# Kernel tuning notes

Hardware: AMD Instinct MI355X
Metric: run time of the kernel (lower is better)

Reference implementation:

```python
import jax, jax.numpy as jnp
import numpy as np

N = 10000   # nodes
E = 100000  # edges
B = 64      # graphs
HID = 128


def setup_inputs() -> dict:
    key = jax.random.key(0)
    ks = iter(jax.random.split(key, 64))
    def nrm(shape, s=0.1):
        return jax.random.normal(next(ks), shape, dtype=jnp.float32) * s
    inp = {}
    inp["x"] = nrm((N, 1), 1.0)
    inp["node_type"] = jax.random.randint(next(ks), (N,), 0, 2)
    inp["edge_index"] = jax.random.randint(next(ks), (2, E), 0, N)
    inp["edge_attr"] = nrm((E, 1), 1.0)
    inp["batch"] = jnp.sort(jax.random.randint(next(ks), (N,), 0, B))
    inp["vp_w"] = nrm((1, HID)); inp["vp_b"] = nrm((HID,))
    inp["type_emb"] = nrm((2, HID))
    def conv(pre, fin, h, c):
        inp[pre + "_wl"] = nrm((fin, h * c)); inp[pre + "_bl"] = nrm((h * c,))
        inp[pre + "_wr"] = nrm((fin, h * c)); inp[pre + "_br"] = nrm((h * c,))
        inp[pre + "_we"] = nrm((1, h * c));  inp[pre + "_att"] = nrm((h, c))
        inp[pre + "_bias"] = nrm((h * c if pre != "c3" else c,))
    conv("c1", HID, 8, HID)
    conv("c2", HID * 8, 2, HID)
    conv("c3", HID * 2, 1, HID)
    inp["m1_w"] = nrm((HID, HID)); inp["m1_b"] = nrm((HID,))
    inp["ln1_g"] = jnp.ones((HID,), jnp.float32); inp["ln1_b"] = jnp.zeros((HID,), jnp.float32)
    inp["m2_w"] = nrm((HID, HID // 2)); inp["m2_b"] = nrm((HID // 2,))
    inp["ln2_g"] = jnp.ones((HID // 2,), jnp.float32); inp["ln2_b"] = jnp.zeros((HID // 2,), jnp.float32)
    inp["m3_w"] = nrm((HID // 2, 1)); inp["m3_b"] = nrm((1,))
    return inp


def _gatv2(x, src, dst, ea, wl, bl, wr, br, we, att, bias, heads, out_ch, concat):
    """PyG GATv2Conv (eval mode): add self-loops (edge_attr fill='mean' over dst),
    attn = (att * leaky_relu(Wl x_src + Wr x_dst + We e)).sum(-1), segment-softmax
    over destination, scatter-add of alpha * Wl x_src."""
    n = x.shape[0]
    ones = jnp.ones((ea.shape[0], 1), ea.dtype)
    deg = jax.ops.segment_sum(ones, dst, num_segments=n)
    loop_attr = jax.ops.segment_sum(ea, dst, num_segments=n) / jnp.maximum(deg, 1.0)
    ar = jnp.arange(n, dtype=src.dtype)
    src2 = jnp.concatenate([src, ar])
    dst2 = jnp.concatenate([dst, ar])
    ea2 = jnp.concatenate([ea, loop_attr], axis=0)
    xl = (x @ wl + bl).reshape(n, heads, out_ch)   # source transform
    xr = (x @ wr + br).reshape(n, heads, out_ch)   # target transform
    e = (ea2 @ we).reshape(-1, heads, out_ch)      # [E2, H, C]
    msg = xl[src2]                                 # [E2, H, C]
    z = jax.nn.leaky_relu(msg + xr[dst2] + e, 0.2)
    score = jnp.einsum('ehc,hc->eh', z, att)       # [E2, H]
    smax = jax.ops.segment_max(score, dst2, num_segments=n)
    ex = jnp.exp(score - smax[dst2])
    denom = jax.ops.segment_sum(ex, dst2, num_segments=n)
    alpha = ex / denom[dst2]
    out = jax.ops.segment_sum(alpha[:, :, None] * msg, dst2, num_segments=n)
    out = out.reshape(n, heads * out_ch) if concat else out.mean(axis=1)
    return out + bias


def _layernorm(v, g, b):
    mu = v.mean(-1, keepdims=True)
    var = v.var(-1, keepdims=True)
    return (v - mu) / jnp.sqrt(var + 1e-5) * g + b


def reference(x, node_type, edge_index, edge_attr, batch,
              vp_w, vp_b, type_emb,
              c1_wl, c1_bl, c1_wr, c1_br, c1_we, c1_att, c1_bias,
              c2_wl, c2_bl, c2_wr, c2_br, c2_we, c2_att, c2_bias,
              c3_wl, c3_bl, c3_wr, c3_br, c3_we, c3_att, c3_bias,
              m1_w, m1_b, ln1_g, ln1_b, m2_w, m2_b, ln2_g, ln2_b, m3_w, m3_b):
    src, dst = edge_index[0], edge_index[1]
    h = x @ vp_w + vp_b + type_emb[node_type]
    h = jax.nn.leaky_relu(_gatv2(h, src, dst, edge_attr, c1_wl, c1_bl, c1_wr, c1_br, c1_we, c1_att, c1_bias, 8, HID, True), 0.2)
    h = jax.nn.leaky_relu(_gatv2(h, src, dst, edge_attr, c2_wl, c2_bl, c2_wr, c2_br, c2_we, c2_att, c2_bias, 2, HID, True), 0.2)
    h = jax.nn.leaky_relu(_gatv2(h, src, dst, edge_attr, c3_wl, c3_bl, c3_wr, c3_br, c3_we, c3_att, c3_bias, 1, HID, False), 0.2)
    # masked global mean pool over node_type == 0
    w = (node_type == 0).astype(h.dtype)
    sums = jax.ops.segment_sum(h * w[:, None], batch, num_segments=B)
    cnts = jax.ops.segment_sum(w, batch, num_segments=B)
    pooled = sums / jnp.maximum(cnts, 1.0)[:, None]
    h1 = jax.nn.leaky_relu(_layernorm(pooled @ m1_w + m1_b, ln1_g, ln1_b), 0.2)
    h2 = jax.nn.leaky_relu(_layernorm(h1 @ m2_w + m2_b, ln2_g, ln2_b), 0.2)
    return (h2 @ m3_w + m3_b).squeeze(-1)
```

## Files before the change

### kernel.cpp

```cpp
#include <hip/hip_runtime.h>
#include <math.h>

#define NN 10000
#define NE 100000
#define NBATCH 64

typedef short bf16x8 __attribute__((ext_vector_type(8)));
typedef float f32x4 __attribute__((ext_vector_type(4)));

__device__ __forceinline__ float lrelu(float v){ return v > 0.f ? v : 0.2f*v; }

__device__ __forceinline__ unsigned short f2bf(float x){
  unsigned int u = __float_as_uint(x);
  u += 0x7fffu + ((u >> 16) & 1u);
  return (unsigned short)(u >> 16);
}
__device__ __forceinline__ float bf2f(unsigned short u){
  return __uint_as_float(((unsigned int)u) << 16);
}

__global__ __launch_bounds__(256) void prep_kernel(
    const float* __restrict__ vp_w, const float* __restrict__ vp_b,
    const float* __restrict__ type_emb,
    const float* __restrict__ c1_wl, const float* __restrict__ c1_bl,
    const float* __restrict__ c1_wr, const float* __restrict__ c1_br,
    float* __restrict__ Ul, float* __restrict__ CTl,
    float* __restrict__ Ur, float* __restrict__ CTr,
    const float* __restrict__ c2_wl, const float* __restrict__ c2_wr,
    const float* __restrict__ c3_wl, const float* __restrict__ c3_wr,
    unsigned short* __restrict__ W2lT, unsigned short* __restrict__ W2rT,
    unsigned short* __restrict__ W3lT, unsigned short* __restrict__ W3rT,
    float* __restrict__ zbase, int zero_words)
{
  __shared__ float t[64][65];
  int b = blockIdx.x;
  int tid = threadIdx.x;
  if (b < 144){
    const float* in; unsigned short* out; int K, N, idx;
    if (b < 64)      { in=c2_wl; out=W2lT; K=1024; N=256; idx=b; }
    else if (b <128) { in=c2_wr; out=W2rT; K=1024; N=256; idx=b-64; }
    else if (b <136) { in=c3_wl; out=W3lT; K=256;  N=128; idx=b-128; }
    else             { in=c3_wr; out=W3rT; K=256;  N=128; idx=b-136; }
    int K64 = K >> 6;
    int kx = idx % K64, nx = idx / K64;
    int k0 = kx*64, n0 = nx*64;
    int lr = tid >> 4;
    int lc = (tid & 15) * 4;
#pragma unroll
    for (int i=0;i<4;++i){
      int r = lr + i*16;
      float4 v = *(const float4*)(in + (size_t)(k0+r)*N + n0 + lc);
      t[r][lc+0]=v.x; t[r][lc+1]=v.y; t[r][lc+2]=v.z; t[r][lc+3]=v.w;
    }
    __syncthreads();
    int sr = tid >> 3;
    int sc = (tid & 7) * 8;
#pragma unroll
    for (int i=0;i<2;++i){
      int n = sr + i*32;
      unsigned short tmp[8];
#pragma unroll
      for (int j=0;j<8;++j) tmp[j] = f2bf(t[sc+j][n]);
      unsigned short* op = out + (size_t)(n0+n)*K + k0 + sc;
      *(ushort4*)op       = make_ushort4(tmp[0],tmp[1],tmp[2],tmp[3]);
      *(ushort4*)(op + 4) = make_ushort4(tmp[4],tmp[5],tmp[6],tmp[7]);
    }
  } else if (b < 148){
    int j = (b-144)*256 + tid;
    float ul=0.f, c0l=0.f, c1l=0.f, ur=0.f, c0r=0.f, c1r=0.f;
    for (int k=0; k<128; ++k){
      float a = c1_wl[k*1024 + j], bb = c1_wr[k*1024 + j];
      float vw = vp_w[k], vb = vp_b[k], t0 = type_emb[k], t1 = type_emb[128+k];
      ul += vw*a; ur += vw*bb;
      c0l += (vb+t0)*a; c1l += (vb+t1)*a;
      c0r += (vb+t0)*bb; c1r += (vb+t1)*bb;
    }
    Ul[j]=ul; Ur[j]=ur;
    CTl[j]      = c0l + c1_bl[j];
    CTl[1024+j] = c1l + c1_bl[j];
    CTr[j]      = c0r + c1_br[j];
    CTr[1024+j] = c1r + c1_br[j];
  } else {
    for (int i = (b-148)*256 + tid; i < zero_words; i += 32*256)
      zbase[i] = 0.f;
  }
}

__global__ __launch_bounds__(1024) void csr_kernel(
    const int* __restrict__ src, const int* __restrict__ dst, const float* __restrict__ ea,
    int* __restrict__ deg, float* __restrict__ loop_sum,
    int* __restrict__ rowptr, float* __restrict__ loop_attr,
    int* __restrict__ rowctr, int* __restrict__ srcs, float* __restrict__ eav,
    int* __restrict__ sync_)
{
  int tid = threadIdx.x;
  int e = blockIdx.x*1024 + tid;
  int d_ = 0; float eav_ = 0.f;
  bool active = e < NE;
  if (active){
    d_ = dst[e]; eav_ = ea[e];
    atomicAdd(&deg[d_], 1);
    atomicAdd(&loop_sum[d_], eav_);
  }
  __threadfence();
  __syncthreads();
  __shared__ int amlast;
  if (tid == 0) amlast = (atomicAdd(&sync_[0], 1) == (int)gridDim.x - 1);
  __syncthreads();
  if (amlast){
    __shared__ int wsum[16];
    __shared__ int carry_s;
    int lane = tid & 63, wid = tid >> 6;
    if (tid == 0) carry_s = 0;
    __syncthreads();
    for (int base = 0; base < NN; base += 1024){
      int i = base + tid;
      int v = 0; float ls = 0.f;
      if (i < NN){ v = atomicAdd(&deg[i], 0); ls = atomicAdd(&loop_sum[i], 0.f); }
      int incl = v;
#pragma unroll
      for (int off=1; off<64; off<<=1){
        int tt = __shfl_up(incl, off, 64);
        if (lane >= off) incl += tt;
      }
      if (lane == 63) wsum[wid] = incl;
      __syncthreads();
      int pre = carry_s;
      for (int w2=0; w2<wid; ++w2) pre += wsum[w2];
      if (i < NN){
        rowptr[i] = pre + incl - v;
        loop_attr[i] = ls / fmaxf((float)v, 1.f);
      }
      __syncthreads();
      if (tid == 0){
        int t2 = 0;
        for (int w2=0; w2<16; ++w2) t2 += wsum[w2];
        carry_s += t2;
      }
      __syncthreads();
    }
    if (tid == 0) rowptr[NN] = carry_s;
    __threadfence();
    __syncthreads();
    if (tid == 0) atomicExch(&sync_[1], 1);
  }
  if (tid == 0){
    while (atomicAdd(&sync_[1], 0) == 0) __builtin_amdgcn_s_sleep(16);
  }
  __syncthreads();
  if (active){
    int p = atomicAdd(&rowptr[d_], 0) + atomicAdd(&rowctr[d_], 1);
    srcs[p] = src[e];
    eav[p] = eav_;
  }
}

__global__ __launch_bounds__(256) void conv1_kernel(
    const int* __restrict__ rowptr, const int* __restrict__ srcs, const float* __restrict__ eav,
    const float* __restrict__ loop_attr, const float* __restrict__ x, const int* __restrict__ ntype,
    const float* __restrict__ Ul, const float* __restrict__ CTl,
    const float* __restrict__ Ur, const float* __restrict__ CTr,
    const float* __restrict__ we, const float* __restrict__ att, const float* __restrict__ bias,
    unsigned short* __restrict__ out)
{
  int n = blockIdx.x;
  int tid = threadIdx.x;
  int ch0 = tid * 4;
  float wev[4], atv[4], biv[4], ulv[4], c0l[4], c1l[4], xrv[4];
  {
    float urv[4], c0r[4], c1r[4];
#pragma unroll
    for (int v=0; v<4; ++v){
      int ch = ch0 + v;
      wev[v] = we[ch]; atv[v] = att[ch]; biv[v] = bias[ch];
      ulv[v] = Ul[ch]; c0l[v] = CTl[ch]; c1l[v] = CTl[1024+ch];
      urv[v] = Ur[ch]; c0r[v] = CTr[ch]; c1r[v] = CTr[1024+ch];
    }
    float xn = x[n];
    int tn = ntype[n];
#pragma unroll
    for (int v=0; v<4; ++v) xrv[v] = xn*urv[v] + (tn ? c1r[v] : c0r[v]);
  }
  float m0=-INFINITY, l0=0.f, A0[4]={0.f,0.f,0.f,0.f};
  float m1=-INFINITY, l1=0.f, A1[4]={0.f,0.f,0.f,0.f};
  int beg = rowptr[n], end = rowptr[n+1];
  for (int j = beg; j <= end; j += 2){
    bool two = (j+1) <= end;
    int s0 = (j < end) ? srcs[j] : n;
    float e0 = (j < end) ? eav[j] : loop_attr[n];
    int s1 = n; float e1 = 0.f;
    if (two){ s1 = (j+1 < end) ? srcs[j+1] : n; e1 = (j+1 < end) ? eav[j+1] : loop_attr[n]; }
    float xs0 = x[s0]; int ts0 = ntype[s0];
    float xs1 = 0.f; int ts1 = 0;
    if (two){ xs1 = x[s1]; ts1 = ntype[s1]; }
    float xl0[4], xl1[4];
#pragma unroll
    for (int v=0; v<4; ++v){
      xl0[v] = xs0*ulv[v] + (ts0 ? c1l[v] : c0l[v]);
      xl1[v] = xs1*ulv[v] + (ts1 ? c1l[v] : c0l[v]);
    }
    float p0 = 0.f, p1 = 0.f;
#pragma unroll
    for (int v=0; v<4; ++v){
      p0 += atv[v]*lrelu(xl0[v] + xrv[v] + e0*wev[v]);
      p1 += atv[v]*lrelu(xl1[v] + xrv[v] + e1*wev[v]);
    }
#pragma unroll
    for (int mm=1; mm<32; mm<<=1){
      p0 += __shfl_xor(p0, mm, 64);
      p1 += __shfl_xor(p1, mm, 64);
    }
    {
      float mn = fmaxf(m0, p0), sc = __expf(m0-mn), pe = __expf(p0-mn);
      l0 = l0*sc + pe; m0 = mn;
#pragma unroll
      for (int v=0; v<4; ++v) A0[v] = A0[v]*sc + pe*xl0[v];
    }
    if (two){
      float mn = fmaxf(m1, p1), sc = __expf(m1-mn), pe = __expf(p1-mn);
      l1 = l1*sc + pe; m1 = mn;
#pragma unroll
      for (int v=0; v<4; ++v) A1[v] = A1[v]*sc + pe*xl1[v];
    }
  }
  float mn = fmaxf(m0, m1);
  float sc0 = __expf(m0-mn), sc1 = __expf(m1-mn);
  float inv = 1.f/(l0*sc0 + l1*sc1);
  size_t baseo = (size_t)n*1024 + ch0;
  ushort4 o;
  o.x = f2bf(lrelu((A0[0]*sc0 + A1[0]*sc1)*inv + biv[0]));
  o.y = f2bf(lrelu((A0[1]*sc0 + A1[1]*sc1)*inv + biv[1]));
  o.z = f2bf(lrelu((A0[2]*sc0 + A1[2]*sc1)*inv + biv[2]));
  o.w = f2bf(lrelu((A0[3]*sc0 + A1[3]*sc1)*inv + biv[3]));
  *(ushort4*)(out + baseo) = o;
}

template<int H, int THREADS, int VPT, bool ONLY0, bool OUTBF, bool INBF>
__global__ __launch_bounds__(THREADS) void conv_kernel(
    const int* __restrict__ rowptr, const int* __restrict__ srcs, const float* __restrict__ eav,
    const float* __restrict__ loop_attr, const int* __restrict__ ntype,
    const void* __restrict__ Xv, int stride, int xr_off,
    const float* __restrict__ we, const float* __restrict__ att, const float* __restrict__ bias,
    void* __restrict__ out)
{
  const int HC = THREADS*VPT;
  const int TPH = THREADS/H;
  int n = blockIdx.x;
  if (ONLY0 && ntype[n] != 0) return;
  int tid = threadIdx.x;
  int ch0 = tid * VPT;
  const float* Xf = (const float*)Xv;
  const unsigned short* Xb = (const unsigned short*)Xv;
  float wev[VPT], atv[VPT], biv[VPT], xrv[VPT];
#pragma unroll
  for (int v=0; v<VPT; ++v){
    int ch = ch0+v;
    wev[v]=we[ch]; atv[v]=att[ch]; biv[v]=bias[ch];
  }
  if constexpr (INBF){
    ushort4 q = *(const ushort4*)(Xb + (size_t)n*stride + xr_off + ch0);
    xrv[0]=bf2f(q.x); xrv[1]=bf2f(q.y); xrv[2]=bf2f(q.z); xrv[3]=bf2f(q.w);
  } else {
#pragma unroll
    for (int v=0; v<VPT; ++v) xrv[v]=Xf[(size_t)n*stride + xr_off + ch0+v];
  }
  float m0=-INFINITY, l0=0.f, A0[VPT];
  float m1=-INFINITY, l1=0.f, A1[VPT];
#pragma unroll
  for (int v=0; v<VPT; ++v){ A0[v]=0.f; A1[v]=0.f; }
  int beg=rowptr[n], end=rowptr[n+1];
  for (int j=beg; j<=end; j+=2){
    bool two = (j+1) <= end;
    int s0 = (j < end) ? srcs[j] : n;
    float e0 = (j < end) ? eav[j] : loop_attr[n];
    int s1 = n; float e1 = 0.f;
    if (two){ s1 = (j+1 < end) ? srcs[j+1] : n; e1 = (j+1 < end) ? eav[j+1] : loop_attr[n]; }
    float x0[VPT], x1[VPT];
    if constexpr (INBF){
      ushort4 q0 = *(const ushort4*)(Xb + (size_t)s0*stride + ch0);
      x0[0]=bf2f(q0.x); x0[1]=bf2f(q0.y); x0[2]=bf2f(q0.z); x0[3]=bf2f(q0.w);
      if (two){
        ushort4 q1 = *(const ushort4*)(Xb + (size_t)s1*stride + ch0);
        x1[0]=bf2f(q1.x); x1[1]=bf2f(q1.y); x1[2]=bf2f(q1.z); x1[3]=bf2f(q1.w);
      } else { x1[0]=x1[1]=x1[2]=x1[3]=0.f; }
    } else if constexpr (VPT == 4){
      float4 q0 = *(const float4*)(Xf + (size_t)s0*stride + ch0);
      x0[0]=q0.x; x0[1]=q0.y; x0[2]=q0.z; x0[3]=q0.w;
      if (two){
        float4 q1 = *(const float4*)(Xf + (size_t)s1*stride + ch0);
        x1[0]=q1.x; x1[1]=q1.y; x1[2]=q1.z; x1[3]=q1.w;
      } else { x1[0]=x1[1]=x1[2]=x1[3]=0.f; }
    } else {
      float2 q0 = *(const float2*)(Xf + (size_t)s0*stride + ch0);
      x0[0]=q0.x; x0[1]=q0.y;
      if (two){
        float2 q1 = *(const float2*)(Xf + (size_t)s1*stride + ch0);
        x1[0]=q1.x; x1[1]=q1.y;
      } else { x1[0]=x1[1]=0.f; }
    }
    float p0=0.f, p1=0.f;
#pragma unroll
    for (int v=0; v<VPT; ++v){
      p0 += atv[v]*lrelu(x0[v]+xrv[v]+e0*wev[v]);
      p1 += atv[v]*lrelu(x1[v]+xrv[v]+e1*wev[v]);
    }
#pragma unroll
    for (int mm=1; mm<TPH; mm<<=1){
      p0 += __shfl_xor(p0, mm, 64);
      p1 += __shfl_xor(p1, mm, 64);
    }
    {
      float mn=fmaxf(m0,p0), sc=__expf(m0-mn), pe=__expf(p0-mn);
      l0=l0*sc+pe; m0=mn;
#pragma unroll
      for (int v=0; v<VPT; ++v) A0[v]=A0[v]*sc+pe*x0[v];
    }
    if (two){
      float mn=fmaxf(m1,p1), sc=__expf(m1-mn), pe=__expf(p1-mn);
      l1=l1*sc+pe; m1=mn;
#pragma unroll
      for (int v=0; v<VPT; ++v) A1[v]=A1[v]*sc+pe*x1[v];
    }
  }
  float mn = fmaxf(m0, m1);
  float sc0 = __expf(m0-mn), sc1 = __expf(m1-mn);
  float inv = 1.f/(l0*sc0 + l1*sc1);
  size_t baseo=(size_t)n*HC+ch0;
  if constexpr (OUTBF){
    unsigned short* ob = (unsigned short*)out;
    ushort4 o;
    o.x = f2bf(lrelu((A0[0]*sc0+A1[0]*sc1)*inv+biv[0]));
    o.y = f2bf(lrelu((A0[1]*sc0+A1[1]*sc1)*inv+biv[1]));
    o.z = f2bf(lrelu((A0[2]*sc0+A1[2]*sc1)*inv+biv[2]));
    o.w = f2bf(lrelu((A0[3]*sc0+A1[3]*sc1)*inv+biv[3]));
    *(ushort4*)(ob + baseo) = o;
  } else {
    float* of = (float*)out;
#pragma unroll
    for (int v=0; v<VPT; ++v) of[baseo+v]=lrelu((A0[v]*sc0+A1[v]*sc1)*inv+biv[v]);
  }
}

template<bool OUTBF>
__global__ __launch_bounds__(256) void gemm_dual_lds(
    const short* __restrict__ Abf,
    const short* __restrict__ WlT, const short* __restrict__ WrT,
    const float* __restrict__ bl, const float* __restrict__ br,
    void* __restrict__ Out, int M, int K, int NcH, int cgrid, int rgrid)
{
  __shared__ short lds[12288];
  int id = blockIdx.x;
  int xcd = id & 7, slot = id >> 3;
  int nb = slot % cgrid;
  int rowgroup = (slot / cgrid) * 8 + xcd;
  if (rowgroup >= rgrid) return;
  int row0 = rowgroup * 128;
  int NC2 = 2*NcH;
  int halfx = NcH >> 6;
  int isR = nb >= halfx;
  const short* WT = isR ? WrT : WlT;
  const float* bias = isR ? br : bl;
  int col0 = (nb - (isR ? halfx : 0)) * 64;
  int gcol0 = nb * 64;
  int tid = threadIdx.x;
  int lane = tid & 63, wave = tid >> 6;
  int wm = wave >> 1, wn = wave & 1;
  int quad = lane >> 4, l16 = lane & 15;

  const short* asrc[4];
#pragma unroll
  for (int i=0;i<4;++i){
    int c = wave*256 + i*64 + lane;
    int m = c >> 3, j = c & 7;
    int gr = row0 + m; gr = gr < M ? gr : M-1;
    asrc[i] = Abf + (size_t)gr*K + ((j ^ (m & 7)) << 3);
  }
  const short* bsrc[2];
#pragma unroll
  for (int i=0;i<2;++i){
    int c = wave*128 + i*64 + lane;
    int nloc = c >> 3, j = c & 7;
    bsrc[i] = WT + (size_t)(col0 + nloc)*K + ((j ^ (nloc & 7)) << 3);
  }

  float biasv[2] = { bias[col0 + wn*32 + l16], bias[col0 + wn*32 + 16 + l16] };
  f32x4 acc[4][2];
#pragma unroll
  for (int f=0; f<4; ++f)
#pragma unroll
    for (int g=0; g<2; ++g) acc[f][g] = (f32x4){0.f,0.f,0.f,0.f};

  int niter = K >> 6;
  for (int it=0; it<niter; ++it){
    int k0 = it << 6;
#pragma unroll
    for (int i=0;i<4;++i)
      __builtin_amdgcn_global_load_lds(asrc[i] + k0, &lds[(wave*256 + i*64)*8], 16, 0, 0);
#pragma unroll
    for (int i=0;i<2;++i)
      __builtin_amdgcn_global_load_lds(bsrc[i] + k0, &lds[8192 + (wave*128 + i*64)*8], 16, 0, 0);
    __syncthreads();
#pragma unroll
    for (int s=0; s<2; ++s){
      int t = s*4 + quad;
      bf16x8 af[4], bfv[2];
#pragma unroll
      for (int f=0; f<4; ++f){
        int m = wm*64 + f*16 + l16;
        af[f] = *(const bf16x8*)&lds[m*64 + ((t ^ (m & 7)) << 3)];
      }
#pragma unroll
      for (int g=0; g<2; ++g){
        int nloc = wn*32 + g*16 + l16;
        bfv[g] = *(const bf16x8*)&lds[8192 + nloc*64 + ((t ^ (nloc & 7)) << 3)];
      }
#pragma unroll
      for (int f=0; f<4; ++f)
#pragma unroll
        for (int g=0; g<2; ++g)
          acc[f][g] = __builtin_amdgcn_mfma_f32_16x16x32_bf16(af[f], bfv[g], acc[f][g], 0,0,0);
    }
    __syncthreads();
  }

#pragma unroll
  for (int f=0; f<4; ++f){
    int rbase = row0 + wm*64 + f*16 + quad*4;
#pragma unroll
    for (int r=0; r<4; ++r){
      int rr = rbase + r;
      if (rr < M){
#pragma unroll
        for (int g=0; g<2; ++g){
          int cc = gcol0 + wn*32 + g*16 + l16;
          float val = acc[f][g][r] + biasv[g];
          if constexpr (OUTBF) ((unsigned short*)Out)[(size_t)rr*NC2 + cc] = f2bf(val);
          else                 ((float*)Out)[(size_t)rr*NC2 + cc] = val;
        }
      }
    }
  }
}

__device__ __forceinline__ int lbound(const int* __restrict__ a, int n, int key){
  int lo = 0, hi = n;
  while (lo < hi){ int mid = (lo+hi) >> 1; if (a[mid] < key) lo = mid+1; else hi = mid; }
  return lo;
}

__global__ __launch_bounds__(128) void head_kernel(
    const float* __restrict__ h3, const int* __restrict__ ntype, const int* __restrict__ batch,
    const float* __restrict__ m1w, const float* __restrict__ m1b,
    const float* __restrict__ g1, const float* __restrict__ b1,
    const float* __restrict__ m2w, const float* __restrict__ m2b,
    const float* __restrict__ g2, const float* __restrict__ b2,
    const float* __restrict__ m3w, const float* __restrict__ m3b,
    float* __restrict__ out)
{
  __shared__ float p[128];
  __shared__ float hb[128];
  __shared__ float red[128];
  int b = blockIdx.x, j = threadIdx.x;
  int lo = lbound(batch, NN, b);
  int hi = lbound(batch, NN, b+1);
  float s = 0.f, cnt = 0.f;
  int n = lo;
  for (; n + 3 < hi; n += 4){
    float w0 = (ntype[n]   == 0) ? 1.f : 0.f;
    float w1 = (ntype[n+1] == 0) ? 1.f : 0.f;
    float w2 = (ntype[n+2] == 0) ? 1.f : 0.f;
    float w3 = (ntype[n+3] == 0) ? 1.f : 0.f;
    s += w0*h3[(size_t)n*128 + j]     + w1*h3[(size_t)(n+1)*128 + j]
       + w2*h3[(size_t)(n+2)*128 + j] + w3*h3[(size_t)(n+3)*128 + j];
    cnt += w0 + w1 + w2 + w3;
  }
  for (; n < hi; ++n){
    float w = (ntype[n] == 0) ? 1.f : 0.f;
    s += w*h3[(size_t)n*128 + j];
    cnt += w;
  }
  p[j] = s / fmaxf(cnt, 1.f);
  __syncthreads();
  float a = m1b[j];
  for (int k=0; k<128; ++k) a += p[k]*m1w[k*128 + j];
  red[j] = a; __syncthreads();
  for (int off=64; off>0; off>>=1){ if (j<off) red[j] += red[j+off]; __syncthreads(); }
  float mu = red[0] * (1.f/128.f);
  __syncthreads();
  float d = a - mu;
  red[j] = d*d; __syncthreads();
  for (int off=64; off>0; off>>=1){ if (j<off) red[j] += red[j+off]; __syncthreads(); }
  float var = red[0] * (1.f/128.f);
  __syncthreads();
  hb[j] = lrelu(d * rsqrtf(var + 1e-5f) * g1[j] + b1[j]);
  __syncthreads();
  float a2 = 0.f;
  if (j < 64){
    a2 = m2b[j];
    for (int k=0; k<128; ++k) a2 += hb[k]*m2w[k*64 + j];
  }
  red[j] = (j<64) ? a2 : 0.f; __syncthreads();
  for (int off=64; off>0; off>>=1){ if (j<off) red[j] += red[j+off]; __syncthreads(); }
  float mu2 = red[0] * (1.f/64.f);
  __syncthreads();
  float d2 = a2 - mu2;
  red[j] = (j<64) ? d2*d2 : 0.f; __syncthreads();
  for (int off=64; off>0; off>>=1){ if (j<off) red[j] += red[j+off]; __syncthreads(); }
  float var2 = red[0] * (1.f/64.f);
  __syncthreads();
  if (j < 64) hb[j] = lrelu(d2 * rsqrtf(var2 + 1e-5f) * g2[j] + b2[j]);
  __syncthreads();
  if (j == 0){
    float o = m3b[0];
    for (int k=0; k<64; ++k) o += hb[k]*m3w[k];
    out[b] = o;
  }
}

extern "C" void kernel_launch(void* const* d_in, const int* in_sizes, int n_in,
                              void* d_out, int out_size, void* d_ws, size_t ws_size,
                              hipStream_t stream)
{
  const float* x        = (const float*)d_in[0];
  const int*   ntype    = (const int*)d_in[1];
  const int*   ei       = (const int*)d_in[2];
  const float* eattr    = (const float*)d_in[3];
  const int*   batch    = (const int*)d_in[4];
  const float* vp_w     = (const float*)d_in[5];
  const float* vp_b     = (const float*)d_in[6];
  const float* type_emb = (const float*)d_in[7];
  const float* c1_wl = (const float*)d_in[8];  const float* c1_bl = (const float*)d_in[9];
  const float* c1_wr = (const float*)d_in[10]; const float* c1_br = (const float*)d_in[11];
  const float* c1_we = (const float*)d_in[12]; const float* c1_att= (const float*)d_in[13];
  const float* c1_bias=(const float*)d_in[14];
  const float* c2_wl = (const float*)d_in[15]; const float* c2_bl = (const float*)d_in[16];
  const float* c2_wr = (const float*)d_in[17]; const float* c2_br = (const float*)d_in[18];
  const float* c2_we = (const float*)d_in[19]; const float* c2_att= (const float*)d_in[20];
  const float* c2_bias=(const float*)d_in[21];
  const float* c3_wl = (const float*)d_in[22]; const float* c3_bl = (const float*)d_in[23];
  const float* c3_wr = (const float*)d_in[24]; const float* c3_br = (const float*)d_in[25];
  const float* c3_we = (const float*)d_in[26]; const float* c3_att= (const float*)d_in[27];
  const float* c3_bias=(const float*)d_in[28];
  const float* m1_w = (const float*)d_in[29]; const float* m1_b = (const float*)d_in[30];
  const float* ln1_g= (const float*)d_in[31]; const float* ln1_b= (const float*)d_in[32];
  const float* m2_w = (const float*)d_in[33]; const float* m2_b = (const float*)d_in[34];
  const float* ln2_g= (const float*)d_in[35]; const float* ln2_b= (const float*)d_in[36];
  const float* m3_w = (const float*)d_in[37]; const float* m3_b = (const float*)d_in[38];
  const int* esrc = ei;
  const int* edst = ei + NE;
  float* outp = (float*)d_out;
  (void)in_sizes; (void)n_in; (void)out_size; (void)ws_size;

  char* w = (char*)d_ws;
  auto alloc = [&](size_t bytes) -> void* {
    void* p = (void*)w;
    w += (bytes + 255) & ~(size_t)255;
    return p;
  };
  unsigned short* h1bf = (unsigned short*)alloc((size_t)NN*1024*2);
  unsigned short* X2   = (unsigned short*)alloc((size_t)NN*512*2);
  unsigned short* h2bf = (unsigned short*)alloc((size_t)NN*256*2);
  float* X3   = (float*)alloc((size_t)NN*256*4);
  float* h3   = (float*)alloc((size_t)NN*128*4);
  unsigned short* W2lT = (unsigned short*)alloc((size_t)256*1024*2);
  unsigned short* W2rT = (unsigned short*)alloc((size_t)256*1024*2);
  unsigned short* W3lT = (unsigned short*)alloc((size_t)128*256*2);
  unsigned short* W3rT = (unsigned short*)alloc((size_t)128*256*2);
  float* Ul   = (float*)alloc(1024*4);
  float* CTl  = (float*)alloc(2048*4);
  float* Ur   = (float*)alloc(1024*4);
  float* CTr  = (float*)alloc(2048*4);
  const int zero_words = 3*NN + 2;
  float* zbase = (float*)alloc((size_t)zero_words*4);
  int*   deg      = (int*)zbase;
  int*   rowctr   = (int*)(zbase + NN);
  float* loop_sum = zbase + 2*NN;
  int*   sync_    = (int*)(zbase + 3*NN);
  float* loop_attr= (float*)alloc((size_t)NN*4);
  int*   rowptr   = (int*)alloc((size_t)(NN+1)*4);
  int*   srcs     = (int*)alloc((size_t)NE*4);
  float* eav      = (float*)alloc((size_t)NE*4);

  prep_kernel<<<180, 256, 0, stream>>>(vp_w, vp_b, type_emb,
      c1_wl, c1_bl, c1_wr, c1_br, Ul, CTl, Ur, CTr,
      c2_wl, c2_wr, c3_wl, c3_wr, W2lT, W2rT, W3lT, W3rT,
      zbase, zero_words);
  csr_kernel<<<(NE+1023)/1024, 1024, 0, stream>>>(esrc, edst, eattr,
      deg, loop_sum, rowptr, loop_attr, rowctr, srcs, eav, sync_);
  conv1_kernel<<<NN, 256, 0, stream>>>(rowptr, srcs, eav, loop_attr, x, ntype,
                                       Ul, CTl, Ur, CTr, c1_we, c1_att, c1_bias, h1bf);
  gemm_dual_lds<true><<<640, 256, 0, stream>>>(
      (const short*)h1bf, (const short*)W2lT, (const short*)W2rT, c2_bl, c2_br,
      (void*)X2, NN, 1024, 256, 8, 79);
  conv_kernel<2,64,4,false,true,true><<<NN, 64, 0, stream>>>(rowptr, srcs, eav, loop_attr, ntype,
      (const void*)X2, 512, 256, c2_we, c2_att, c2_bias, h2bf);
  gemm_dual_lds<false><<<320, 256, 0, stream>>>(
      (const short*)h2bf, (const short*)W3lT, (const short*)W3rT, c3_bl, c3_br,
      (void*)X3, NN, 256, 128, 4, 79);
  conv_kernel<1,64,2,true,false,false><<<NN, 64, 0, stream>>>(rowptr, srcs, eav, loop_attr, ntype,
      (const void*)X3, 256, 128, c3_we, c3_att, c3_bias, h3);
  head_kernel<<<NBATCH, 128, 0, stream>>>(h3, ntype, batch, m1_w, m1_b, ln1_g, ln1_b,
                                          m2_w, m2_b, ln2_g, ln2_b, m3_w, m3_b, outp);
}
```

Baseline: 359.1 us.

## Split conv1 into edge-parallel scoring and per-node softmax aggregation using rank-one structure

Conv1 is split into two kernels. The first computes attention scores for every edge (self-loops included) in an edge-parallel grid, using a precomputed 4-way node-type constant table held in LDS. The second does the per-node, per-head softmax over scalar scores only. Because the first-layer input features are rank-one plus a type constant, the weighted sum reduces to three scalars (sum of alpha times x, and alpha mass per type), which then expand to 1024 channels. This removes the serial per-edge channel loop and its cross-wave reductions, at the cost of writing and reading a 110k×8 score buffer and an extra launch.

```diff
diff --git a/kernel.cpp b/kernel.cpp
--- a/kernel.cpp
+++ b/kernel.cpp
@@ -3,6 +3,7 @@
 
 #define NN 10000
 #define NE 100000
+#define E2 (NE + NN)
 #define NBATCH 64
 
 typedef short bf16x8 __attribute__((ext_vector_type(8)));
@@ -25,7 +26,7 @@
     const float* __restrict__ c1_wl, const float* __restrict__ c1_bl,
     const float* __restrict__ c1_wr, const float* __restrict__ c1_br,
     float* __restrict__ Ul, float* __restrict__ CTl,
-    float* __restrict__ Ur, float* __restrict__ CTr,
+    float* __restrict__ Ur, float* __restrict__ CT2,
     const float* __restrict__ c2_wl, const float* __restrict__ c2_wr,
     const float* __restrict__ c3_wl, const float* __restrict__ c3_wr,
     unsigned short* __restrict__ W2lT, unsigned short* __restrict__ W2rT,
@@ -75,11 +76,14 @@
       c0l += (vb+t0)*a; c1l += (vb+t1)*a;
       c0r += (vb+t0)*bb; c1r += (vb+t1)*bb;
     }
+    float bl = c1_bl[j], br = c1_br[j];
     Ul[j]=ul; Ur[j]=ur;
-    CTl[j]      = c0l + c1_bl[j];
-    CTl[1024+j] = c1l + c1_bl[j];
-    CTr[j]      = c0r + c1_br[j];
-    CTr[1024+j] = c1r + c1_br[j];
+    CTl[j]      = c0l + bl;
+    CTl[1024+j] = c1l + bl;
+    CT2[j]        = (c0l+bl) + (c0r+br);
+    CT2[1024+j]   = (c0l+bl) + (c1r+br);
+    CT2[2048+j]   = (c1l+bl) + (c0r+br);
+    CT2[3072+j]   = (c1l+bl) + (c1r+br);
   } else {
     for (int i = (b-148)*256 + tid; i < zero_words; i += 32*256)
       zbase[i] = 0.f;
@@ -90,8 +94,8 @@
     const int* __restrict__ src, const int* __restrict__ dst, const float* __restrict__ ea,
     int* __restrict__ deg, float* __restrict__ loop_sum,
     int* __restrict__ rowptr, float* __restrict__ loop_attr,
-    int* __restrict__ rowctr, int* __restrict__ srcs, float* __restrict__ eav,
-    int* __restrict__ sync_)
+    int* __restrict__ rowctr, int* __restrict__ srcs, int* __restrict__ dsts,
+    float* __restrict__ eav, int* __restrict__ sync_)
 {
   int tid = threadIdx.x;
   int e = blockIdx.x*1024 + tid;
@@ -151,88 +155,96 @@
   if (active){
     int p = atomicAdd(&rowptr[d_], 0) + atomicAdd(&rowctr[d_], 1);
     srcs[p] = src[e];
+    dsts[p] = d_;
     eav[p] = eav_;
   }
 }
 
-__global__ __launch_bounds__(256) void conv1_kernel(
-    const int* __restrict__ rowptr, const int* __restrict__ srcs, const float* __restrict__ eav,
+__global__ __launch_bounds__(256) void conv1_score(
+    const int* __restrict__ srcs, const int* __restrict__ dsts, const float* __restrict__ eav,
     const float* __restrict__ loop_attr, const float* __restrict__ x, const int* __restrict__ ntype,
+    const float* __restrict__ Ul, const float* __restrict__ Ur, const float* __restrict__ CT2,
+    const float* __restrict__ we, const float* __restrict__ att,
+    float* __restrict__ scores)
+{
+  __shared__ float ldsct[4096];
+  int tid = threadIdx.x;
+  for (int i = tid; i < 1024; i += 256)
+    *(float4*)&ldsct[i*4] = *(const float4*)&CT2[i*4];
+  int te = tid & 127;
+  int sub = tid >> 7;
+  int ch0 = te * 8;
+  float ul[8], ur[8], wev[8], atv[8];
+#pragma unroll
+  for (int v=0; v<8; ++v){
+    ul[v]=Ul[ch0+v]; ur[v]=Ur[ch0+v]; wev[v]=we[ch0+v]; atv[v]=att[ch0+v];
+  }
+  __syncthreads();
+  for (int j = blockIdx.x*2 + sub; j < E2; j += gridDim.x*2){
+    int s, d; float ea;
+    if (j < NE){ s = srcs[j]; d = dsts[j]; ea = eav[j]; }
+    else       { s = j - NE;  d = s;       ea = loop_attr[s]; }
+    float xs = x[s], xn = x[d];
+    int tt = ntype[s]*2 + ntype[d];
+    const float* cp = &ldsct[tt*1024 + ch0];
+    float4 c0 = *(const float4*)cp;
+    float4 c1 = *(const float4*)(cp+4);
+    float ct[8] = {c0.x,c0.y,c0.z,c0.w,c1.x,c1.y,c1.z,c1.w};
+    float p = 0.f;
+#pragma unroll
+    for (int v=0; v<8; ++v){
+      float z = fmaf(xs, ul[v], fmaf(xn, ur[v], fmaf(ea, wev[v], ct[v])));
+      p += atv[v]*lrelu(z);
+    }
+#pragma unroll
+    for (int mm=1; mm<16; mm<<=1) p += __shfl_xor(p, mm, 16);
+    if ((te & 15) == 0) scores[(size_t)j*8 + (te>>4)] = p;
+  }
+}
+
+__global__ __launch_bounds__(256) void conv1_agg(
+    const int* __restrict__ rowptr, const int* __restrict__ srcs,
+    const float* __restrict__ scores, const float* __restrict__ x, const int* __restrict__ ntype,
     const float* __restrict__ Ul, const float* __restrict__ CTl,
-    const float* __restrict__ Ur, const float* __restrict__ CTr,
-    const float* __restrict__ we, const float* __restrict__ att, const float* __restrict__ bias,
-    unsigned short* __restrict__ out)
+    const float* __restrict__ bias, unsigned short* __restrict__ out)
 {
   int n = blockIdx.x;
   int tid = threadIdx.x;
+  int h = tid >> 5, el = tid & 31;
+  int beg = rowptr[n], deg = rowptr[n+1] - beg;
+  int cnt = deg + 1;
+  float m = -1e30f, l = 0.f, s1 = 0.f, s20 = 0.f;
+  for (int i = el; i < cnt; i += 32){
+    int pos; int s;
+    if (i < deg){ pos = beg + i; s = srcs[pos]; }
+    else        { pos = NE + n;  s = n; }
+    float p = scores[(size_t)pos*8 + h];
+    float xs = x[s];
+    float w0 = (ntype[s] == 0) ? 1.f : 0.f;
+    float mn = fmaxf(m, p), f = __expf(m-mn), pe = __expf(p-mn);
+    l = l*f + pe; s1 = s1*f + pe*xs; s20 = s20*f + pe*w0; m = mn;
+  }
+#pragma unroll
+  for (int off=1; off<32; off<<=1){
+    float mb = __shfl_xor(m, off, 32), lb = __shfl_xor(l, off, 32);
+    float s1b = __shfl_xor(s1, off, 32), s20b = __shfl_xor(s20, off, 32);
+    float mn = fmaxf(m, mb), fa = __expf(m-mn), fb = __expf(mb-mn);
+    l = l*fa + lb*fb; s1 = s1*fa + s1b*fb; s20 = s20*fa + s20b*fb; m = mn;
+  }
+  float inv = 1.f/l;
+  s1 *= inv; s20 *= inv;
+  float s21 = 1.f - s20;
   int ch0 = tid * 4;
-  float wev[4], atv[4], biv[4], ulv[4], c0l[4], c1l[4], xrv[4];
-  {
-    float urv[4], c0r[4], c1r[4];
-#pragma unroll
-    for (int v=0; v<4; ++v){
-      int ch = ch0 + v;
-      wev[v] = we[ch]; atv[v] = att[ch]; biv[v] = bias[ch];
-      ulv[v] = Ul[ch]; c0l[v] = CTl[ch]; c1l[v] = CTl[1024+ch];
-      urv[v] = Ur[ch]; c0r[v] = CTr[ch]; c1r[v] = CTr[1024+ch];
-    }
-    float xn = x[n];
-    int tn = ntype[n];
-#pragma unroll
-    for (int v=0; v<4; ++v) xrv[v] = xn*urv[v] + (tn ? c1r[v] : c0r[v]);
-  }
-  float m0=-INFINITY, l0=0.f, A0[4]={0.f,0.f,0.f,0.f};
-  float m1=-INFINITY, l1=0.f, A1[4]={0.f,0.f,0.f,0.f};
-  int beg = rowptr[n], end = rowptr[n+1];
-  for (int j = beg; j <= end; j += 2){
-    bool two = (j+1) <= end;
-    int s0 = (j < end) ? srcs[j] : n;
-    float e0 = (j < end) ? eav[j] : loop_attr[n];
-    int s1 = n; float e1 = 0.f;
-    if (two){ s1 = (j+1 < end) ? srcs[j+1] : n; e1 = (j+1 < end) ? eav[j+1] : loop_attr[n]; }
-    float xs0 = x[s0]; int ts0 = ntype[s0];
-    float xs1 = 0.f; int ts1 = 0;
-    if (two){ xs1 = x[s1]; ts1 = ntype[s1]; }
-    float xl0[4], xl1[4];
-#pragma unroll
-    for (int v=0; v<4; ++v){
-      xl0[v] = xs0*ulv[v] + (ts0 ? c1l[v] : c0l[v]);
-      xl1[v] = xs1*ulv[v] + (ts1 ? c1l[v] : c0l[v]);
-    }
-    float p0 = 0.f, p1 = 0.f;
-#pragma unroll
-    for (int v=0; v<4; ++v){
-      p0 += atv[v]*lrelu(xl0[v] + xrv[v] + e0*wev[v]);
-      p1 += atv[v]*lrelu(xl1[v] + xrv[v] + e1*wev[v]);
-    }
-#pragma unroll
-    for (int mm=1; mm<32; mm<<=1){
-      p0 += __shfl_xor(p0, mm, 64);
-      p1 += __shfl_xor(p1, mm, 64);
-    }
-    {
-      float mn = fmaxf(m0, p0), sc = __expf(m0-mn), pe = __expf(p0-mn);
-      l0 = l0*sc + pe; m0 = mn;
-#pragma unroll
-      for (int v=0; v<4; ++v) A0[v] = A0[v]*sc + pe*xl0[v];
-    }
-    if (two){
-      float mn = fmaxf(m1, p1), sc = __expf(m1-mn), pe = __expf(p1-mn);
-      l1 = l1*sc + pe; m1 = mn;
-#pragma unroll
-      for (int v=0; v<4; ++v) A1[v] = A1[v]*sc + pe*xl1[v];
-    }
-  }
-  float mn = fmaxf(m0, m1);
-  float sc0 = __expf(m0-mn), sc1 = __expf(m1-mn);
-  float inv = 1.f/(l0*sc0 + l1*sc1);
-  size_t baseo = (size_t)n*1024 + ch0;
+  float4 u  = *(const float4*)(Ul + ch0);
+  float4 t0 = *(const float4*)(CTl + ch0);
+  float4 t1 = *(const float4*)(CTl + 1024 + ch0);
+  float4 bi = *(const float4*)(bias + ch0);
   ushort4 o;
-  o.x = f2bf(lrelu((A0[0]*sc0 + A1[0]*sc1)*inv + biv[0]));
-  o.y = f2bf(lrelu((A0[1]*sc0 + A1[1]*sc1)*inv + biv[1]));
-  o.z = f2bf(lrelu((A0[2]*sc0 + A1[2]*sc1)*inv + biv[2]));
-  o.w = f2bf(lrelu((A0[3]*sc0 + A1[3]*sc1)*inv + biv[3]));
-  *(ushort4*)(out + baseo) = o;
+  o.x = f2bf(lrelu(s1*u.x + s20*t0.x + s21*t1.x + bi.x));
+  o.y = f2bf(lrelu(s1*u.y + s20*t0.y + s21*t1.y + bi.y));
+  o.z = f2bf(lrelu(s1*u.z + s20*t0.z + s21*t1.z + bi.z));
+  o.w = f2bf(lrelu(s1*u.w + s20*t0.w + s21*t1.w + bi.w));
+  *(ushort4*)(out + (size_t)n*1024 + ch0) = o;
 }
 
 template<int H, int THREADS, int VPT, bool ONLY0, bool OUTBF, bool INBF>
@@ -569,7 +581,8 @@
   float* Ul   = (float*)alloc(1024*4);
   float* CTl  = (float*)alloc(2048*4);
   float* Ur   = (float*)alloc(1024*4);
-  float* CTr  = (float*)alloc(2048*4);
+  float* CT2  = (float*)alloc(4096*4);
+  float* scores = (float*)alloc((size_t)E2*8*4);
   const int zero_words = 3*NN + 2;
   float* zbase = (float*)alloc((size_t)zero_words*4);
   int*   deg      = (int*)zbase;
@@ -579,16 +592,19 @@
   float* loop_attr= (float*)alloc((size_t)NN*4);
   int*   rowptr   = (int*)alloc((size_t)(NN+1)*4);
   int*   srcs     = (int*)alloc((size_t)NE*4);
+  int*   dsts     = (int*)alloc((size_t)NE*4);
   float* eav      = (float*)alloc((size_t)NE*4);
 
   prep_kernel<<<180, 256, 0, stream>>>(vp_w, vp_b, type_emb,
-      c1_wl, c1_bl, c1_wr, c1_br, Ul, CTl, Ur, CTr,
+      c1_wl, c1_bl, c1_wr, c1_br, Ul, CTl, Ur, CT2,
       c2_wl, c2_wr, c3_wl, c3_wr, W2lT, W2rT, W3lT, W3rT,
       zbase, zero_words);
   csr_kernel<<<(NE+1023)/1024, 1024, 0, stream>>>(esrc, edst, eattr,
-      deg, loop_sum, rowptr, loop_attr, rowctr, srcs, eav, sync_);
-  conv1_kernel<<<NN, 256, 0, stream>>>(rowptr, srcs, eav, loop_attr, x, ntype,
-                                       Ul, CTl, Ur, CTr, c1_we, c1_att, c1_bias, h1bf);
+      deg, loop_sum, rowptr, loop_attr, rowctr, srcs, dsts, eav, sync_);
+  conv1_score<<<2048, 256, 0, stream>>>(srcs, dsts, eav, loop_attr, x, ntype,
+      Ul, Ur, CT2, c1_we, c1_att, scores);
+  conv1_agg<<<NN, 256, 0, stream>>>(rowptr, srcs, scores, x, ntype,
+      Ul, CTl, c1_bias, h1bf);
   gemm_dual_lds<true><<<640, 256, 0, stream>>>(
       (const short*)h1bf, (const short*)W2lT, (const short*)W2rT, c2_bl, c2_br,
       (void*)X2, NN, 1024, 256, 8, 79);
```

Measured after the change: 347.4 us. -3.3%, faster.
